# Optimization experiments

Hardware: AMD Instinct MI355X
Metric: run time of the kernel (lower is better)

## Reference

```python
import jax, jax.numpy as jnp
import numpy as np

B, T, C = 4, 2048, 1024
H = 16
HD = C // H  # 64


def setup_inputs() -> dict:
    key = jax.random.key(0)
    ks = jax.random.split(key, 5)
    x = jax.random.normal(ks[0], (B, T, C), dtype=jnp.float32)
    # torch nn.Linear weights have shape [out_features, in_features]
    s = 1.0 / np.sqrt(C)
    Wq = jax.random.uniform(ks[1], (C, C), jnp.float32, -s, s)
    Wk = jax.random.uniform(ks[2], (C, C), jnp.float32, -s, s)
    Wv = jax.random.uniform(ks[3], (C, C), jnp.float32, -s, s)
    Wo = jax.random.uniform(ks[4], (C, C), jnp.float32, -s, s)
    return {"x": x, "Wq": Wq, "Wk": Wk, "Wv": Wv, "Wo": Wo}


def _split_heads(t):
    b, s, c = t.shape
    return t.reshape(b, s, H, HD).transpose(0, 2, 1, 3)  # [B,H,T,HD]


def reference(x, Wq, Wk, Wv, Wo):
    q = _split_heads(x @ Wq.T)
    k = _split_heads(x @ Wk.T)
    v = _split_heads(x @ Wv.T)
    scale = 1.0 / np.sqrt(HD).astype(np.float32)
    scores = jnp.einsum('bhqd,bhkd->bhqk', q, k) * scale  # [B,H,T,T]
    causal = jnp.tril(jnp.ones((T, T), dtype=bool))
    scores = jnp.where(causal[None, None], scores, -jnp.inf)
    weights = jax.nn.softmax(scores, axis=-1)
    ctx = jnp.einsum('bhqk,bhkd->bhqd', weights, v)
    y = ctx.transpose(0, 2, 1, 3).reshape(x.shape[0], x.shape[1], C)
    return y @ Wo.T
```

## Files before the change

### kernel.cpp

```cpp
#include <hip/hip_runtime.h>

typedef __attribute__((ext_vector_type(8))) short short8;
typedef __attribute__((ext_vector_type(4))) float floatx4;

__device__ __forceinline__ ushort f2bf(float f) {
  unsigned u = __float_as_uint(f);
  u += 0x7fffu + ((u >> 16) & 1u);
  return (ushort)(u >> 16);
}

__device__ __forceinline__ uint2 pack4(floatx4 v, float scale) {
  unsigned p0 = __float_as_uint(v[0] * scale) + 0x8000u;
  unsigned p1 = __float_as_uint(v[1] * scale) + 0x8000u;
  unsigned p2 = __float_as_uint(v[2] * scale) + 0x8000u;
  unsigned p3 = __float_as_uint(v[3] * scale) + 0x8000u;
  uint2 w;
  w.x = __builtin_amdgcn_perm(p1, p0, 0x07060302);
  w.y = __builtin_amdgcn_perm(p3, p2, 0x07060302);
  return w;
}

__device__ __forceinline__ void gll16(const ushort* g, ushort* l) {
  __builtin_amdgcn_global_load_lds(
      (const __attribute__((address_space(1))) unsigned int*)(g),
      (__attribute__((address_space(3))) unsigned int*)(l), 16, 0, 0);
}

__global__ void cvt_bf16(const float* __restrict__ in, ushort* __restrict__ out, int n) {
  int i = (blockIdx.x * blockDim.x + threadIdx.x) * 4;
  if (i >= n) return;
  float4 v = *(const float4*)(in + i);
  ushort4 o = make_ushort4(f2bf(v.x), f2bf(v.y), f2bf(v.z), f2bf(v.w));
  *(ushort4*)(out + i) = o;
}

__global__ void cvt_w4(const float* __restrict__ a, const float* __restrict__ b,
                       const float* __restrict__ c, const float* __restrict__ d,
                       ushort* __restrict__ oa, ushort* __restrict__ ob,
                       ushort* __restrict__ oc, ushort* __restrict__ od) {
  int which = blockIdx.x >> 10;
  const float* in = which == 0 ? a : (which == 1 ? b : (which == 2 ? c : d));
  ushort* out = which == 0 ? oa : (which == 1 ? ob : (which == 2 ? oc : od));
  int i = ((blockIdx.x & 1023) * 256 + threadIdx.x) * 4;
  float4 v = *(const float4*)(in + i);
  ushort4 o = make_ushort4(f2bf(v.x), f2bf(v.y), f2bf(v.z), f2bf(v.w));
  *(ushort4*)(out + i) = o;
}

__global__ __launch_bounds__(256) void gemm_qk(const ushort* __restrict__ A,
                                               const ushort* __restrict__ W0,
                                               const ushort* __restrict__ W1,
                                               ushort* __restrict__ Qb,
                                               ushort* __restrict__ Kb) {
  __shared__ __align__(16) ushort sA[128 * 32];
  __shared__ __align__(16) ushort sB[128 * 32];
  const int K = 1024;
  int tid = threadIdx.x, wave = tid >> 6, lane = tid & 63;
  int ln = lane & 15, quad = lane >> 4;
  int m0 = blockIdx.y * 128;
  int n0g = blockIdx.x * 128;
  int mat = n0g >> 10;
  int n0 = n0g & 1023;
  const ushort* Bw = mat == 0 ? W0 : W1;
  int la = lane >> 2, lk = (lane & 3) * 8;

  floatx4 acc[4][4];
  for (int i = 0; i < 4; i++)
    for (int t = 0; t < 4; t++) acc[i][t] = (floatx4)0.0f;
  int mrow = (wave >> 1) * 64, ncol = (wave & 1) * 64;

  for (int k0 = 0; k0 < K; k0 += 32) {
    __syncthreads();
    for (int c = 0; c < 2; c++) {
      int chunk = wave * 2 + c;
      gll16(&A[(size_t)(m0 + chunk * 16 + la) * K + k0 + lk], &sA[chunk * 512]);
      gll16(&Bw[(size_t)(n0 + chunk * 16 + la) * K + k0 + lk], &sB[chunk * 512]);
    }
    __syncthreads();
    short8 af[4], bf[4];
    for (int i = 0; i < 4; i++) af[i] = *(const short8*)&sB[(ncol + i * 16 + ln) * 32 + quad * 8];
    for (int t = 0; t < 4; t++) bf[t] = *(const short8*)&sA[(mrow + t * 16 + ln) * 32 + quad * 8];
    for (int i = 0; i < 4; i++)
      for (int t = 0; t < 4; t++)
        acc[i][t] = __builtin_amdgcn_mfma_f32_16x16x32_bf16(af[i], bf[t], acc[i][t], 0, 0, 0);
  }

  float qs = (mat == 0) ? 0.18033688f : 1.0f;
  ushort* dst = (mat == 0) ? Qb : Kb;
  for (int i = 0; i < 4; i++) {
    for (int t = 0; t < 4; t++) {
      int n = n0 + ncol + i * 16 + quad * 4;
      int m = m0 + mrow + t * 16 + ln;
      int b = m >> 11, tt = m & 2047, h = n >> 6, hd = n & 63;
      *(uint2*)&dst[((((size_t)b * 16 + h) * 2048 + tt) << 6) + hd] = pack4(acc[i][t], qs);
    }
  }
}

__global__ __launch_bounds__(256) void gemm_v(const ushort* __restrict__ A,
                                              const ushort* __restrict__ W2,
                                              ushort* __restrict__ VT) {
  __shared__ __align__(16) ushort sA[128 * 32];
  __shared__ __align__(16) ushort sB[128 * 32];
  const int K = 1024;
  int tid = threadIdx.x, wave = tid >> 6, lane = tid & 63;
  int ln = lane & 15, quad = lane >> 4;
  int m0 = blockIdx.y * 128;
  int n0 = blockIdx.x * 128;
  int la = lane >> 2, lk = (lane & 3) * 8;

  floatx4 acc[4][4];
  for (int i = 0; i < 4; i++)
    for (int t = 0; t < 4; t++) acc[i][t] = (floatx4)0.0f;
  int mrow = (wave >> 1) * 64, ncol = (wave & 1) * 64;

  for (int k0 = 0; k0 < K; k0 += 32) {
    __syncthreads();
    for (int c = 0; c < 2; c++) {
      int chunk = wave * 2 + c;
      gll16(&A[(size_t)(m0 + chunk * 16 + la) * K + k0 + lk], &sA[chunk * 512]);
      gll16(&W2[(size_t)(n0 + chunk * 16 + la) * K + k0 + lk], &sB[chunk * 512]);
    }
    __syncthreads();
    short8 af[4], bf[4];
    for (int i = 0; i < 4; i++) af[i] = *(const short8*)&sA[(mrow + i * 16 + ln) * 32 + quad * 8];
    for (int t = 0; t < 4; t++) bf[t] = *(const short8*)&sB[(ncol + t * 16 + ln) * 32 + quad * 8];
    for (int i = 0; i < 4; i++)
      for (int t = 0; t < 4; t++)
        acc[i][t] = __builtin_amdgcn_mfma_f32_16x16x32_bf16(af[i], bf[t], acc[i][t], 0, 0, 0);
  }

  for (int i = 0; i < 4; i++) {
    for (int t = 0; t < 4; t++) {
      int m = m0 + mrow + i * 16 + quad * 4;
      int n = n0 + ncol + t * 16 + ln;
      int b = m >> 11, tt = m & 2047, h = n >> 6, hd = n & 63;
      *(uint2*)&VT[(((size_t)b * 16 + h) * 64 + hd) * 2048 + tt] = pack4(acc[i][t], 1.0f);
    }
  }
}

__global__ __launch_bounds__(256) void gemm_out(const ushort* __restrict__ A,
                                                const ushort* __restrict__ W0,
                                                float* __restrict__ Fout) {
  __shared__ __align__(16) ushort sA[128 * 32];
  __shared__ __align__(16) ushort sB[128 * 32];
  const int K = 1024;
  int tid = threadIdx.x, wave = tid >> 6, lane = tid & 63;
  int ln = lane & 15, quad = lane >> 4;
  int m0 = blockIdx.y * 128;
  int n0 = blockIdx.x * 128;
  int la = lane >> 2, lk = (lane & 3) * 8;

  floatx4 acc[4][4];
  for (int i = 0; i < 4; i++)
    for (int t = 0; t < 4; t++) acc[i][t] = (floatx4)0.0f;
  int mrow = (wave >> 1) * 64, ncol = (wave & 1) * 64;

  for (int k0 = 0; k0 < K; k0 += 32) {
    __syncthreads();
    for (int c = 0; c < 2; c++) {
      int chunk = wave * 2 + c;
      gll16(&A[(size_t)(m0 + chunk * 16 + la) * K + k0 + lk], &sA[chunk * 512]);
      gll16(&W0[(size_t)(n0 + chunk * 16 + la) * K + k0 + lk], &sB[chunk * 512]);
    }
    __syncthreads();
    short8 af[4], bf[4];
    for (int i = 0; i < 4; i++) af[i] = *(const short8*)&sB[(ncol + i * 16 + ln) * 32 + quad * 8];
    for (int t = 0; t < 4; t++) bf[t] = *(const short8*)&sA[(mrow + t * 16 + ln) * 32 + quad * 8];
    for (int i = 0; i < 4; i++)
      for (int t = 0; t < 4; t++)
        acc[i][t] = __builtin_amdgcn_mfma_f32_16x16x32_bf16(af[i], bf[t], acc[i][t], 0, 0, 0);
  }

  for (int i = 0; i < 4; i++) {
    for (int t = 0; t < 4; t++) {
      int n = n0 + ncol + i * 16 + quad * 4;
      int m = m0 + mrow + t * 16 + ln;
      *(floatx4*)&Fout[(size_t)m * 1024 + n] = acc[i][t];
    }
  }
}

#define SD 76
__global__ __launch_bounds__(256) void attn(const ushort* __restrict__ Qb,
                                            const ushort* __restrict__ Kb,
                                            const ushort* __restrict__ VTb,
                                            ushort* __restrict__ ctx) {
  __shared__ __align__(16) ushort sK[64 * SD];
  __shared__ __align__(16) ushort sVT[64 * SD];
  __shared__ __align__(16) ushort sP[128 * SD];

  int tid = threadIdx.x, wave = tid >> 6, lane = tid & 63;
  int ln = lane & 15, quad = lane >> 4;
  int bh = blockIdx.x;
  int qb = 15 - blockIdx.y;

  const ushort* Qp = Qb + (size_t)bh * 2048 * 64 + (size_t)qb * 128 * 64;
  const ushort* Kp = Kb + (size_t)bh * 2048 * 64;
  const ushort* VTp = VTb + (size_t)bh * 64 * 2048;

  for (int i = 0; i < 4; i++) {
    int e = tid + i * 256;
    int row = e >> 3, c8 = (e & 7) * 8;
    *(uint4*)&sP[row * SD + c8] = *(const uint4*)&Qp[row * 64 + c8];
  }
  __syncthreads();
  short8 qf[2][2];
  for (int f = 0; f < 2; f++)
    for (int ks = 0; ks < 2; ks++)
      qf[f][ks] = *(const short8*)&sP[(wave * 32 + f * 16 + ln) * SD + ks * 32 + quad * 8];

  floatx4 o[2][4];
  for (int f = 0; f < 2; f++)
    for (int t = 0; t < 4; t++) o[f][t] = (floatx4)0.0f;
  float l_acc[2] = {0.0f, 0.0f};

  int kt_m = 2 * qb + (wave >> 1);
  int ktend = 2 * qb + 1;

  for (int kt = 0; kt <= ktend; kt++) {
    __syncthreads();
    for (int i = 0; i < 2; i++) {
      int e = tid + i * 256;
      int row = e >> 3, c8 = (e & 7) * 8;
      *(uint4*)&sK[row * SD + c8] = *(const uint4*)&Kp[(size_t)(kt * 64 + row) * 64 + c8];
      *(uint4*)&sVT[row * SD + c8] = *(const uint4*)&VTp[((size_t)row << 11) + kt * 64 + c8];
    }
    __syncthreads();
    if (kt > kt_m) continue;

    floatx4 s[2][4];
    for (int f = 0; f < 2; f++)
      for (int t = 0; t < 4; t++) s[f][t] = (floatx4)0.0f;
    for (int ks = 0; ks < 2; ks++) {
      short8 kf[4];
      for (int t = 0; t < 4; t++)
        kf[t] = *(const short8*)&sK[(t * 16 + ln) * SD + ks * 32 + quad * 8];
      for (int f = 0; f < 2; f++)
        for (int t = 0; t < 4; t++)
          s[f][t] = __builtin_amdgcn_mfma_f32_16x16x32_bf16(kf[t], qf[f][ks], s[f][t], 0, 0, 0);
    }

    if (kt == kt_m) {
      for (int f = 0; f < 2; f++) {
        int qg = qb * 128 + wave * 32 + f * 16 + ln;
        for (int t = 0; t < 4; t++) {
          int kg = kt * 64 + t * 16 + quad * 4;
          for (int r = 0; r < 4; r++)
            if (kg + r > qg) s[f][t][r] = -1e30f;
        }
      }
    }

    for (int f = 0; f < 2; f++) {
      int prow = (wave * 32 + f * 16 + ln) * SD;
      for (int t = 0; t < 4; t++) {
        floatx4 p;
        for (int r = 0; r < 4; r++) {
          p[r] = __builtin_amdgcn_exp2f(s[f][t][r]);
          l_acc[f] += p[r];
        }
        *(uint2*)&sP[prow + t * 16 + quad * 4] = pack4(p, 1.0f);
      }
    }

    for (int ks = 0; ks < 2; ks++) {
      short8 vf[4];
      for (int t = 0; t < 4; t++)
        vf[t] = *(const short8*)&sVT[(t * 16 + ln) * SD + ks * 32 + quad * 8];
      for (int f = 0; f < 2; f++) {
        short8 pf = *(const short8*)&sP[(wave * 32 + f * 16 + ln) * SD + ks * 32 + quad * 8];
        for (int t = 0; t < 4; t++)
          o[f][t] = __builtin_amdgcn_mfma_f32_16x16x32_bf16(pf, vf[t], o[f][t], 0, 0, 0);
      }
    }
  }

  for (int f = 0; f < 2; f++) {
    l_acc[f] += __shfl_xor(l_acc[f], 16);
    l_acc[f] += __shfl_xor(l_acc[f], 32);
  }

  int b = bh >> 4, h = bh & 15;
  for (int f = 0; f < 2; f++) {
    for (int r = 0; r < 4; r++) {
      float lr = __shfl(l_acc[f], quad * 4 + r);
      float linv = 1.0f / lr;
      int qg = qb * 128 + wave * 32 + f * 16 + quad * 4 + r;
      for (int t = 0; t < 4; t++) {
        int col = h * 64 + t * 16 + ln;
        ctx[((size_t)b * 2048 + qg) * 1024 + col] = f2bf(o[f][t][r] * linv);
      }
    }
  }
}

extern "C" void kernel_launch(void* const* d_in, const int* in_sizes, int n_in,
                              void* d_out, int out_size, void* d_ws, size_t ws_size,
                              hipStream_t stream) {
  const float* x  = (const float*)d_in[0];
  const float* Wq = (const float*)d_in[1];
  const float* Wk = (const float*)d_in[2];
  const float* Wv = (const float*)d_in[3];
  const float* Wo = (const float*)d_in[4];
  float* out = (float*)d_out;

  char* ws = (char*)d_ws;
  const size_t MB = 1024 * 1024;
  ushort* xb   = (ushort*)(ws + 0);
  ushort* Wqb  = (ushort*)(ws + 16 * MB);
  ushort* Wkb  = (ushort*)(ws + 18 * MB);
  ushort* Wvb  = (ushort*)(ws + 20 * MB);
  ushort* Wob  = (ushort*)(ws + 22 * MB);
  ushort* Qb   = (ushort*)(ws + 24 * MB);
  ushort* Kb   = (ushort*)(ws + 40 * MB);
  ushort* Vtb  = (ushort*)(ws + 56 * MB);
  ushort* ctxb = xb;

  cvt_bf16<<<8192, 256, 0, stream>>>(x, xb, 8388608);
  cvt_w4<<<4096, 256, 0, stream>>>(Wq, Wk, Wv, Wo, Wqb, Wkb, Wvb, Wob);

  gemm_qk<<<dim3(16, 64), 256, 0, stream>>>(xb, Wqb, Wkb, Qb, Kb);
  gemm_v<<<dim3(8, 64), 256, 0, stream>>>(xb, Wvb, Vtb);
  attn<<<dim3(64, 16), 256, 0, stream>>>(Qb, Kb, Vtb, ctxb);
  gemm_out<<<dim3(8, 64), 256, 0, stream>>>(ctxb, Wob, out);
}
```

Baseline: 292.5 us.

## Double GEMM K-tile to 64 with XOR-swizzled LDS and async attention loads

The three projection GEMMs now stage 64-wide K tiles per barrier pair instead of 32, halving the number of synchronisations per output tile. LDS rows are XOR-swizzled to avoid bank conflicts on the fragment reads. The attention kernel's K/V tile staging switches from register-mediated copies to direct global-to-LDS loads with the same swizzle. The two conversion kernels are merged into a single launch. LDS use per GEMM block doubles, which may lower occupancy.

```diff
diff --git a/kernel.cpp b/kernel.cpp
--- a/kernel.cpp
+++ b/kernel.cpp
@@ -26,25 +26,37 @@
       (__attribute__((address_space(3))) unsigned int*)(l), 16, 0, 0);
 }
 
-__global__ void cvt_bf16(const float* __restrict__ in, ushort* __restrict__ out, int n) {
-  int i = (blockIdx.x * blockDim.x + threadIdx.x) * 4;
-  if (i >= n) return;
+__global__ void cvt_all(const float* __restrict__ x, const float* __restrict__ a,
+                        const float* __restrict__ b, const float* __restrict__ c,
+                        const float* __restrict__ d, ushort* __restrict__ ox,
+                        ushort* __restrict__ oa, ushort* __restrict__ ob,
+                        ushort* __restrict__ oc, ushort* __restrict__ od) {
+  int bid = blockIdx.x;
+  const float* in;
+  ushort* out;
+  int lb;
+  if (bid < 8192) { in = x; out = ox; lb = bid; }
+  else {
+    int w = (bid - 8192) >> 10;
+    lb = (bid - 8192) & 1023;
+    in = w == 0 ? a : (w == 1 ? b : (w == 2 ? c : d));
+    out = w == 0 ? oa : (w == 1 ? ob : (w == 2 ? oc : od));
+  }
+  int i = (lb * 256 + threadIdx.x) * 4;
   float4 v = *(const float4*)(in + i);
   ushort4 o = make_ushort4(f2bf(v.x), f2bf(v.y), f2bf(v.z), f2bf(v.w));
   *(ushort4*)(out + i) = o;
 }
 
-__global__ void cvt_w4(const float* __restrict__ a, const float* __restrict__ b,
-                       const float* __restrict__ c, const float* __restrict__ d,
-                       ushort* __restrict__ oa, ushort* __restrict__ ob,
-                       ushort* __restrict__ oc, ushort* __restrict__ od) {
-  int which = blockIdx.x >> 10;
-  const float* in = which == 0 ? a : (which == 1 ? b : (which == 2 ? c : d));
-  ushort* out = which == 0 ? oa : (which == 1 ? ob : (which == 2 ? oc : od));
-  int i = ((blockIdx.x & 1023) * 256 + threadIdx.x) * 4;
-  float4 v = *(const float4*)(in + i);
-  ushort4 o = make_ushort4(f2bf(v.x), f2bf(v.y), f2bf(v.z), f2bf(v.w));
-  *(ushort4*)(out + i) = o;
+__device__ __forceinline__ void stage64(const ushort* __restrict__ G, size_t gstride,
+                                        int grow0, int gcol0, ushort* __restrict__ S,
+                                        int wave, int lane) {
+  int r8 = lane >> 3;
+  int sc = ((lane & 7) ^ (r8 & 7)) * 8;
+  for (int c = 0; c < 4; c++) {
+    int rl = wave * 32 + c * 8;
+    gll16(&G[(size_t)(grow0 + rl + r8) * gstride + gcol0 + sc], &S[rl * 64]);
+  }
 }
 
 __global__ __launch_bounds__(256) void gemm_qk(const ushort* __restrict__ A,
@@ -52,8 +64,8 @@
                                                const ushort* __restrict__ W1,
                                                ushort* __restrict__ Qb,
                                                ushort* __restrict__ Kb) {
-  __shared__ __align__(16) ushort sA[128 * 32];
-  __shared__ __align__(16) ushort sB[128 * 32];
+  __shared__ __align__(16) ushort sA[128 * 64];
+  __shared__ __align__(16) ushort sB[128 * 64];
   const int K = 1024;
   int tid = threadIdx.x, wave = tid >> 6, lane = tid & 63;
   int ln = lane & 15, quad = lane >> 4;
@@ -62,27 +74,26 @@
   int mat = n0g >> 10;
   int n0 = n0g & 1023;
   const ushort* Bw = mat == 0 ? W0 : W1;
-  int la = lane >> 2, lk = (lane & 3) * 8;
 
   floatx4 acc[4][4];
   for (int i = 0; i < 4; i++)
     for (int t = 0; t < 4; t++) acc[i][t] = (floatx4)0.0f;
   int mrow = (wave >> 1) * 64, ncol = (wave & 1) * 64;
 
-  for (int k0 = 0; k0 < K; k0 += 32) {
-    __syncthreads();
-    for (int c = 0; c < 2; c++) {
-      int chunk = wave * 2 + c;
-      gll16(&A[(size_t)(m0 + chunk * 16 + la) * K + k0 + lk], &sA[chunk * 512]);
-      gll16(&Bw[(size_t)(n0 + chunk * 16 + la) * K + k0 + lk], &sB[chunk * 512]);
-    }
-    __syncthreads();
-    short8 af[4], bf[4];
-    for (int i = 0; i < 4; i++) af[i] = *(const short8*)&sB[(ncol + i * 16 + ln) * 32 + quad * 8];
-    for (int t = 0; t < 4; t++) bf[t] = *(const short8*)&sA[(mrow + t * 16 + ln) * 32 + quad * 8];
-    for (int i = 0; i < 4; i++)
-      for (int t = 0; t < 4; t++)
-        acc[i][t] = __builtin_amdgcn_mfma_f32_16x16x32_bf16(af[i], bf[t], acc[i][t], 0, 0, 0);
+  for (int k0 = 0; k0 < K; k0 += 64) {
+    __syncthreads();
+    stage64(A, K, m0, k0, sA, wave, lane);
+    stage64(Bw, K, n0, k0, sB, wave, lane);
+    __syncthreads();
+    for (int ks = 0; ks < 2; ks++) {
+      int cs = ((ks * 4 + quad) ^ (ln & 7)) * 8;
+      short8 af[4], bf[4];
+      for (int i = 0; i < 4; i++) af[i] = *(const short8*)&sB[(ncol + i * 16 + ln) * 64 + cs];
+      for (int t = 0; t < 4; t++) bf[t] = *(const short8*)&sA[(mrow + t * 16 + ln) * 64 + cs];
+      for (int i = 0; i < 4; i++)
+        for (int t = 0; t < 4; t++)
+          acc[i][t] = __builtin_amdgcn_mfma_f32_16x16x32_bf16(af[i], bf[t], acc[i][t], 0, 0, 0);
+    }
   }
 
   float qs = (mat == 0) ? 0.18033688f : 1.0f;
@@ -100,34 +111,33 @@
 __global__ __launch_bounds__(256) void gemm_v(const ushort* __restrict__ A,
                                               const ushort* __restrict__ W2,
                                               ushort* __restrict__ VT) {
-  __shared__ __align__(16) ushort sA[128 * 32];
-  __shared__ __align__(16) ushort sB[128 * 32];
+  __shared__ __align__(16) ushort sA[128 * 64];
+  __shared__ __align__(16) ushort sB[128 * 64];
   const int K = 1024;
   int tid = threadIdx.x, wave = tid >> 6, lane = tid & 63;
   int ln = lane & 15, quad = lane >> 4;
   int m0 = blockIdx.y * 128;
   int n0 = blockIdx.x * 128;
-  int la = lane >> 2, lk = (lane & 3) * 8;
 
   floatx4 acc[4][4];
   for (int i = 0; i < 4; i++)
     for (int t = 0; t < 4; t++) acc[i][t] = (floatx4)0.0f;
   int mrow = (wave >> 1) * 64, ncol = (wave & 1) * 64;
 
-  for (int k0 = 0; k0 < K; k0 += 32) {
-    __syncthreads();
-    for (int c = 0; c < 2; c++) {
-      int chunk = wave * 2 + c;
-      gll16(&A[(size_t)(m0 + chunk * 16 + la) * K + k0 + lk], &sA[chunk * 512]);
-      gll16(&W2[(size_t)(n0 + chunk * 16 + la) * K + k0 + lk], &sB[chunk * 512]);
-    }
-    __syncthreads();
-    short8 af[4], bf[4];
-    for (int i = 0; i < 4; i++) af[i] = *(const short8*)&sA[(mrow + i * 16 + ln) * 32 + quad * 8];
-    for (int t = 0; t < 4; t++) bf[t] = *(const short8*)&sB[(ncol + t * 16 + ln) * 32 + quad * 8];
-    for (int i = 0; i < 4; i++)
-      for (int t = 0; t < 4; t++)
-        acc[i][t] = __builtin_amdgcn_mfma_f32_16x16x32_bf16(af[i], bf[t], acc[i][t], 0, 0, 0);
+  for (int k0 = 0; k0 < K; k0 += 64) {
+    __syncthreads();
+    stage64(A, K, m0, k0, sA, wave, lane);
+    stage64(W2, K, n0, k0, sB, wave, lane);
+    __syncthreads();
+    for (int ks = 0; ks < 2; ks++) {
+      int cs = ((ks * 4 + quad) ^ (ln & 7)) * 8;
+      short8 af[4], bf[4];
+      for (int i = 0; i < 4; i++) af[i] = *(const short8*)&sA[(mrow + i * 16 + ln) * 64 + cs];
+      for (int t = 0; t < 4; t++) bf[t] = *(const short8*)&sB[(ncol + t * 16 + ln) * 64 + cs];
+      for (int i = 0; i < 4; i++)
+        for (int t = 0; t < 4; t++)
+          acc[i][t] = __builtin_amdgcn_mfma_f32_16x16x32_bf16(af[i], bf[t], acc[i][t], 0, 0, 0);
+    }
   }
 
   for (int i = 0; i < 4; i++) {
@@ -143,34 +153,33 @@
 __global__ __launch_bounds__(256) void gemm_out(const ushort* __restrict__ A,
                                                 const ushort* __restrict__ W0,
                                                 float* __restrict__ Fout) {
-  __shared__ __align__(16) ushort sA[128 * 32];
-  __shared__ __align__(16) ushort sB[128 * 32];
+  __shared__ __align__(16) ushort sA[128 * 64];
+  __shared__ __align__(16) ushort sB[128 * 64];
   const int K = 1024;
   int tid = threadIdx.x, wave = tid >> 6, lane = tid & 63;
   int ln = lane & 15, quad = lane >> 4;
   int m0 = blockIdx.y * 128;
   int n0 = blockIdx.x * 128;
-  int la = lane >> 2, lk = (lane & 3) * 8;
 
   floatx4 acc[4][4];
   for (int i = 0; i < 4; i++)
     for (int t = 0; t < 4; t++) acc[i][t] = (floatx4)0.0f;
   int mrow = (wave >> 1) * 64, ncol = (wave & 1) * 64;
 
-  for (int k0 = 0; k0 < K; k0 += 32) {
-    __syncthreads();
-    for (int c = 0; c < 2; c++) {
-      int chunk = wave * 2 + c;
-      gll16(&A[(size_t)(m0 + chunk * 16 + la) * K + k0 + lk], &sA[chunk * 512]);
-      gll16(&W0[(size_t)(n0 + chunk * 16 + la) * K + k0 + lk], &sB[chunk * 512]);
-    }
-    __syncthreads();
-    short8 af[4], bf[4];
-    for (int i = 0; i < 4; i++) af[i] = *(const short8*)&sB[(ncol + i * 16 + ln) * 32 + quad * 8];
-    for (int t = 0; t < 4; t++) bf[t] = *(const short8*)&sA[(mrow + t * 16 + ln) * 32 + quad * 8];
-    for (int i = 0; i < 4; i++)
-      for (int t = 0; t < 4; t++)
-        acc[i][t] = __builtin_amdgcn_mfma_f32_16x16x32_bf16(af[i], bf[t], acc[i][t], 0, 0, 0);
+  for (int k0 = 0; k0 < K; k0 += 64) {
+    __syncthreads();
+    stage64(A, K, m0, k0, sA, wave, lane);
+    stage64(W0, K, n0, k0, sB, wave, lane);
+    __syncthreads();
+    for (int ks = 0; ks < 2; ks++) {
+      int cs = ((ks * 4 + quad) ^ (ln & 7)) * 8;
+      short8 af[4], bf[4];
+      for (int i = 0; i < 4; i++) af[i] = *(const short8*)&sB[(ncol + i * 16 + ln) * 64 + cs];
+      for (int t = 0; t < 4; t++) bf[t] = *(const short8*)&sA[(mrow + t * 16 + ln) * 64 + cs];
+      for (int i = 0; i < 4; i++)
+        for (int t = 0; t < 4; t++)
+          acc[i][t] = __builtin_amdgcn_mfma_f32_16x16x32_bf16(af[i], bf[t], acc[i][t], 0, 0, 0);
+    }
   }
 
   for (int i = 0; i < 4; i++) {
@@ -187,8 +196,8 @@
                                             const ushort* __restrict__ Kb,
                                             const ushort* __restrict__ VTb,
                                             ushort* __restrict__ ctx) {
-  __shared__ __align__(16) ushort sK[64 * SD];
-  __shared__ __align__(16) ushort sVT[64 * SD];
+  __shared__ __align__(16) ushort sK[64 * 64];
+  __shared__ __align__(16) ushort sVT[64 * 64];
   __shared__ __align__(16) ushort sP[128 * SD];
 
   int tid = threadIdx.x, wave = tid >> 6, lane = tid & 63;
@@ -218,14 +227,15 @@
 
   int kt_m = 2 * qb + (wave >> 1);
   int ktend = 2 * qb + 1;
+  int r8 = lane >> 3;
+  int scs = ((lane & 7) ^ (r8 & 7)) * 8;
 
   for (int kt = 0; kt <= ktend; kt++) {
     __syncthreads();
-    for (int i = 0; i < 2; i++) {
-      int e = tid + i * 256;
-      int row = e >> 3, c8 = (e & 7) * 8;
-      *(uint4*)&sK[row * SD + c8] = *(const uint4*)&Kp[(size_t)(kt * 64 + row) * 64 + c8];
-      *(uint4*)&sVT[row * SD + c8] = *(const uint4*)&VTp[((size_t)row << 11) + kt * 64 + c8];
+    for (int c = 0; c < 2; c++) {
+      int rl = wave * 16 + c * 8;
+      gll16(&Kp[(size_t)(kt * 64 + rl + r8) * 64 + scs], &sK[rl * 64]);
+      gll16(&VTp[(size_t)(rl + r8) * 2048 + kt * 64 + scs], &sVT[rl * 64]);
     }
     __syncthreads();
     if (kt > kt_m) continue;
@@ -234,9 +244,10 @@
     for (int f = 0; f < 2; f++)
       for (int t = 0; t < 4; t++) s[f][t] = (floatx4)0.0f;
     for (int ks = 0; ks < 2; ks++) {
+      int cs = ((ks * 4 + quad) ^ (ln & 7)) * 8;
       short8 kf[4];
       for (int t = 0; t < 4; t++)
-        kf[t] = *(const short8*)&sK[(t * 16 + ln) * SD + ks * 32 + quad * 8];
+        kf[t] = *(const short8*)&sK[(t * 16 + ln) * 64 + cs];
       for (int f = 0; f < 2; f++)
         for (int t = 0; t < 4; t++)
           s[f][t] = __builtin_amdgcn_mfma_f32_16x16x32_bf16(kf[t], qf[f][ks], s[f][t], 0, 0, 0);
@@ -266,9 +277,10 @@
     }
 
     for (int ks = 0; ks < 2; ks++) {
+      int cs = ((ks * 4 + quad) ^ (ln & 7)) * 8;
       short8 vf[4];
       for (int t = 0; t < 4; t++)
-        vf[t] = *(const short8*)&sVT[(t * 16 + ln) * SD + ks * 32 + quad * 8];
+        vf[t] = *(const short8*)&sVT[(t * 16 + ln) * 64 + cs];
       for (int f = 0; f < 2; f++) {
         short8 pf = *(const short8*)&sP[(wave * 32 + f * 16 + ln) * SD + ks * 32 + quad * 8];
         for (int t = 0; t < 4; t++)
@@ -318,8 +330,7 @@
   ushort* Vtb  = (ushort*)(ws + 56 * MB);
   ushort* ctxb = xb;
 
-  cvt_bf16<<<8192, 256, 0, stream>>>(x, xb, 8388608);
-  cvt_w4<<<4096, 256, 0, stream>>>(Wq, Wk, Wv, Wo, Wqb, Wkb, Wvb, Wob);
+  cvt_all<<<12288, 256, 0, stream>>>(x, Wq, Wk, Wv, Wo, xb, Wqb, Wkb, Wvb, Wob);
 
   gemm_qk<<<dim3(16, 64), 256, 0, stream>>>(xb, Wqb, Wkb, Qb, Kb);
   gemm_v<<<dim3(8, 64), 256, 0, stream>>>(xb, Wvb, Vtb);
```

Measured after the change: 263.6 us. -9.9%, faster.
